# Kernel tuning notes

Measured on AMD Instinct MI355X. Metric: run time of the kernel, lower is better.

## Reference

```python
import jax, jax.numpy as jnp
import numpy as np
import math

B, T, C, H = 4, 2048, 512, 8
HD = C // H


def make_alibias(block_size, ms):
    # ALiBi-style per-head bias: -m_h * |i - j|, shape [1, H, S, S]
    idx = jnp.arange(block_size)
    dist = jnp.abs(idx[:, None] - idx[None, :]).astype(jnp.float32)  # [S,S]
    return -ms[None, :, None, None] * dist[None, None, :, :]


def setup_inputs() -> dict:
    key = jax.random.key(0)
    k1, k2, k3, k4, k5 = jax.random.split(key, 5)
    x = jax.random.normal(k1, (B, T, C), dtype=jnp.float32)
    Wqkv = jax.random.normal(k2, (C, 3 * C), dtype=jnp.float32) * (1.0 / math.sqrt(C))
    bqkv = jax.random.normal(k3, (3 * C,), dtype=jnp.float32) * 0.02
    Wproj = jax.random.normal(k4, (C, C), dtype=jnp.float32) * (1.0 / math.sqrt(C))
    bproj = jax.random.normal(k5, (C,), dtype=jnp.float32) * 0.02
    ms = jnp.arange(1, H + 1, dtype=jnp.float32) * 0.05
    alibias = make_alibias(T, ms)  # [1,H,T,T]
    return {"x": x, "Wqkv": Wqkv, "bqkv": bqkv, "Wproj": Wproj, "bproj": bproj, "alibias": alibias}


def reference(x, Wqkv, bqkv, Wproj, bproj, alibias):
    Bv, Tv, Cv = x.shape
    qkv = x @ Wqkv + bqkv                      # [B,T,3C]
    q, k, v = jnp.split(qkv, 3, axis=-1)
    # [B,T,C] -> [B,H,T,hd]
    def heads(t):
        return t.reshape(Bv, Tv, H, HD).transpose(0, 2, 1, 3)
    q, k, v = heads(q), heads(k), heads(v)
    att = jnp.einsum('bhqd,bhkd->bhqk', q, k) * (1.0 / math.sqrt(HD))
    att = att + alibias[:, :, :Tv, :Tv]
    att = jax.nn.softmax(att, axis=-1)
    y = jnp.einsum('bhqk,bhkd->bhqd', att, v)  # [B,H,T,hd]
    y = y.transpose(0, 2, 1, 3).reshape(Bv, Tv, Cv)
    return y @ Wproj + bproj
```

## Files before the change

kernel.cpp:

```cpp
#include <hip/hip_runtime.h>
#include <hip/hip_bf16.h>

#define LOG2E 1.4426950408889634f

typedef __attribute__((ext_vector_type(8))) short short8;
typedef __attribute__((ext_vector_type(8))) __bf16 bf16x8;
typedef __attribute__((ext_vector_type(4))) float f32x4;

__device__ __forceinline__ unsigned short f2b(float f){
  unsigned int u = __builtin_bit_cast(unsigned int, f);
  u += 0x7fffu + ((u >> 16) & 1u);
  return (unsigned short)(u >> 16);
}

__device__ __forceinline__ unsigned int cvtpk(float lo, float hi){
  unsigned int r;
  asm("v_cvt_pk_bf16_f32 %0, %1, %2" : "=v"(r) : "v"(lo), "v"(hi));
  return r;
}

__device__ __forceinline__ void gload16(const void* g, void* l){
  __builtin_amdgcn_global_load_lds(
      (const __attribute__((address_space(1))) unsigned int*)g,
      (__attribute__((address_space(3))) unsigned int*)l, 16, 0, 0);
}

__global__ __launch_bounds__(256) void prep_kernel(
    const float* __restrict__ x, const float* __restrict__ Wqkv, const float* __restrict__ Wproj,
    unsigned short* __restrict__ xb, unsigned short* __restrict__ wqkvT, unsigned short* __restrict__ wprojT){
  __shared__ unsigned short T[64][72];
  const int bid = blockIdx.x, tid = threadIdx.x;
  if (bid < 2048){
    size_t i = ((size_t)bid * 256 + tid) * 8;
    float4 a = *(const float4*)(x + i);
    float4 b = *(const float4*)(x + i + 4);
    short8 s;
    s[0]=(short)f2b(a.x); s[1]=(short)f2b(a.y); s[2]=(short)f2b(a.z); s[3]=(short)f2b(a.w);
    s[4]=(short)f2b(b.x); s[5]=(short)f2b(b.y); s[6]=(short)f2b(b.z); s[7]=(short)f2b(b.w);
    *(short8*)(xb + i) = s;
    return;
  }
  const float* in; unsigned short* out; int R, C, bx, by;
  if (bid < 2240){ int t = bid - 2048; bx = t % 24; by = t / 24; in = Wqkv; out = wqkvT; R = 512; C = 1536; }
  else           { int t = bid - 2240; bx = t % 8;  by = t / 8;  in = Wproj; out = wprojT; R = 512; C = 512; }
  const int r0 = by * 64, c0 = bx * 64;
  {
    const int i = tid >> 2, jg = (tid & 3) * 16;
    const float* src = in + (size_t)(r0 + i) * C + c0 + jg;
    #pragma unroll
    for (int e = 0; e < 16; e += 4){
      float4 v = *(const float4*)(src + e);
      T[i][jg + e + 0] = f2b(v.x);
      T[i][jg + e + 1] = f2b(v.y);
      T[i][jg + e + 2] = f2b(v.z);
      T[i][jg + e + 3] = f2b(v.w);
    }
  }
  __syncthreads();
  {
    const int j = tid >> 2, ig = (tid & 3) * 16;
    short8 w0, w1;
    #pragma unroll
    for (int e = 0; e < 8; e++) w0[e] = (short)T[ig + e][j];
    #pragma unroll
    for (int e = 0; e < 8; e++) w1[e] = (short)T[ig + 8 + e][j];
    unsigned short* dst = out + (size_t)(c0 + j) * R + r0 + ig;
    *(short8*)dst = w0;
    *(short8*)(dst + 8) = w1;
  }
}

__global__ __launch_bounds__(256,2) void gemm_qkv_kernel(
    const unsigned short* __restrict__ A,
    const unsigned short* __restrict__ Bt,
    const float* __restrict__ bias,
    unsigned short* __restrict__ Qb,
    unsigned short* __restrict__ Kb,
    unsigned short* __restrict__ VTb,
    float* __restrict__ Mq, float* __restrict__ Mk){
  __shared__ unsigned short As[128*64];
  __shared__ unsigned short Bs[128*64];
  const int tid = threadIdx.x, wid = tid >> 6, lane = tid & 63;
  const int wr = wid >> 1, wc = wid & 1;
  const int fr = lane & 15, fq = lane >> 4;
  const int fr7 = fr & 7;
  const int bm = blockIdx.x * 128, bn = blockIdx.y * 128;
  f32x4 acc[4][4];
  #pragma unroll
  for (int m=0;m<4;m++)
    #pragma unroll
    for (int n=0;n<4;n++) acc[m][n] = (f32x4){0.f,0.f,0.f,0.f};

  for (int k0 = 0; k0 < 512; k0 += 64){
    __syncthreads();
    #pragma unroll
    for (int it=0; it<4; it++){
      const int s = it*256 + tid;
      const int row = s >> 3, c = s & 7;
      const int sc = c ^ (row & 7);
      void* al = (void*)(As + (it*256 + wid*64)*8);
      void* bl = (void*)(Bs + (it*256 + wid*64)*8);
      gload16(A  + (size_t)(bm + row)*512 + k0 + sc*8, al);
      gload16(Bt + (size_t)(bn + row)*512 + k0 + sc*8, bl);
    }
    __syncthreads();
    bf16x8 af[4][2], bfv[4][2];
    #pragma unroll
    for (int m=0;m<4;m++)
      #pragma unroll
      for (int kk=0;kk<2;kk++)
        af[m][kk]  = *(const bf16x8*)&As[(wr*64 + m*16 + fr)*64 + (((kk*4+fq)^fr7)*8)];
    #pragma unroll
    for (int n=0;n<4;n++)
      #pragma unroll
      for (int kk=0;kk<2;kk++)
        bfv[n][kk] = *(const bf16x8*)&Bs[(wc*64 + n*16 + fr)*64 + (((kk*4+fq)^fr7)*8)];
    #pragma unroll
    for (int kk=0;kk<2;kk++)
      #pragma unroll
      for (int m=0;m<4;m++)
        #pragma unroll
        for (int n=0;n<4;n++)
          acc[m][n] = __builtin_amdgcn_mfma_f32_16x16x32_bf16(af[m][kk], bfv[n][kk], acc[m][n], 0,0,0);
  }

  const float SCQ = 0.125f * LOG2E;
  const int colbase = bn + wc*64;
  const int which = colbase >> 9;
  float ss[4][4];
  #pragma unroll
  for (int m=0;m<4;m++)
    #pragma unroll
    for (int g=0;g<4;g++) ss[m][g] = 0.f;

  #pragma unroll
  for (int m=0;m<4;m++){
    const int row0 = bm + wr*64 + m*16 + fq*4;
    const int b_ = row0 >> 11, t_ = row0 & 2047;
    #pragma unroll
    for (int n=0;n<4;n++){
      const int col = colbase + n*16 + fr;
      const int c = col & 511, hh = c >> 6, dd = c & 63;
      const float bv = bias[col];
      if (which == 0){
        #pragma unroll
        for (int g=0; g<4; g++){
          const float v = (acc[m][n][g] + bv) * SCQ;
          ss[m][g] = fmaf(v, v, ss[m][g]);
          Qb[((size_t)(b_*8 + hh)*2048 + t_ + g)*64 + dd] = f2b(v);
        }
      } else if (which == 1){
        #pragma unroll
        for (int g=0; g<4; g++){
          const float v = acc[m][n][g] + bv;
          ss[m][g] = fmaf(v, v, ss[m][g]);
          Kb[((size_t)(b_*8 + hh)*2048 + t_ + g)*64 + dd] = f2b(v);
        }
      } else {
        uint2 pk;
        pk.x = cvtpk(acc[m][n][0] + bv, acc[m][n][1] + bv);
        pk.y = cvtpk(acc[m][n][2] + bv, acc[m][n][3] + bv);
        *(uint2*)&VTb[((size_t)(b_*8 + hh)*64 + dd)*2048 + t_] = pk;
      }
    }
  }

  if (which <= 1){
    #pragma unroll
    for (int m=0;m<4;m++)
      #pragma unroll
      for (int g=0;g<4;g++){
        float s = ss[m][g];
        s += __shfl_xor(s, 1); s += __shfl_xor(s, 2);
        s += __shfl_xor(s, 4); s += __shfl_xor(s, 8);
        ss[m][g] = s;
      }
    float mx = 0.f;
    #pragma unroll
    for (int m=0;m<4;m++)
      #pragma unroll
      for (int g=0;g<4;g++) mx = fmaxf(mx, ss[m][g]);
    mx = fmaxf(mx, __shfl_xor(mx, 16));
    mx = fmaxf(mx, __shfl_xor(mx, 32));
    if (lane == 0){
      const int rowbase = bm + wr*64;
      const int b_ = rowbase >> 11, qc_ = (rowbase >> 6) & 31;
      const int h_ = (colbase >> 6) & 7;
      float* M = which ? Mk : Mq;
      M[(b_*8 + h_)*32 + qc_] = sqrtf(mx) * 1.01f;
    }
  }
}

__global__ __launch_bounds__(256,2) void attn_kernel(
    const unsigned short* __restrict__ Q,
    const unsigned short* __restrict__ K,
    const unsigned short* __restrict__ VT,
    const float* __restrict__ alib,
    const float* __restrict__ Mqa,
    const float* __restrict__ Mka,
    unsigned short* __restrict__ Y){
  __shared__ unsigned short Ks[2][64*64];
  __shared__ unsigned short Vs[2][64*64];
  __shared__ unsigned short Ps[4][16][72];
  __shared__ float MkS[32];
  __shared__ float wred[4];
  __shared__ int lst[32];
  __shared__ int nsh;
  const int tid = threadIdx.x, wid = tid >> 6, lane = tid & 63;
  const int fr = lane & 15, fq = lane >> 4;
  const int fr7 = fr & 7;
  const int id = blockIdx.x;
  const int h = id >> 7, r_ = id & 127, b = r_ >> 5, qc = r_ & 31;
  const int bh = b*8 + h;
  const int q0 = qc*64 + wid*16;
  const unsigned short* Qp = Q  + (size_t)bh * 131072;
  const unsigned short* Kp = K  + (size_t)bh * 131072;
  const unsigned short* Vp = VT + (size_t)bh * 131072;
  const float nmh2 = alib[(size_t)h * 4194304 + 1] * LOG2E;
  const float MqMk0 = Mqa[bh*32 + qc];
  if (tid < 32) MkS[tid] = Mka[bh*32 + tid];

  bf16x8 qf[2];
  #pragma unroll
  for (int kk=0;kk<2;kk++)
    qf[kk] = *(const bf16x8*)(Qp + (size_t)(q0 + fr)*64 + kk*32 + fq*8);

  f32x4 o[4];
  #pragma unroll
  for (int ni=0;ni<4;ni++) o[ni] = (f32x4){0.f,0.f,0.f,0.f};
  float mr = -1e30f, lr = 0.f;
  const float qi = (float)(q0 + fr);
  const float qb = nmh2 * qi;
  f32x4 ka[4];
  #pragma unroll
  for (int ni=0;ni<4;ni++)
    #pragma unroll
    for (int g=0;g<4;g++) ka[ni][g] = nmh2 * (float)(ni*16 + fq*4 + g);

  auto stage = [&](int kt, int buf){
    const int kb = kt * 64;
    #pragma unroll
    for (int it=0; it<2; it++){
      const int s = it*256 + tid;
      const int row = s >> 3, c = s & 7;
      const int sc = c ^ (row & 7);
      gload16(Kp + (size_t)(kb + row)*64 + sc*8, (void*)(Ks[buf] + (it*256 + wid*64)*8));
      gload16(Vp + (size_t)row*2048 + kb + sc*8, (void*)(Vs[buf] + (it*256 + wid*64)*8));
    }
  };

  auto compute = [&](int kt, int buf, bool diag){
    const int kb = kt * 64;
    const unsigned short* KsB = Ks[buf];
    const unsigned short* VsB = Vs[buf];
    bf16x8 kf[4][2], vf[4][2];
    #pragma unroll
    for (int ni=0;ni<4;ni++)
      #pragma unroll
      for (int kk=0;kk<2;kk++){
        const int r = ni*16 + fr;
        const int sw = ((kk*4 + fq) ^ fr7) * 8;
        kf[ni][kk] = *(const bf16x8*)&KsB[r*64 + sw];
        vf[ni][kk] = *(const bf16x8*)&VsB[r*64 + sw];
      }

    f32x4 st[4];
    const f32x4 fz = {0.f,0.f,0.f,0.f};
    #pragma unroll
    for (int ni=0;ni<4;ni++){
      f32x4 t0 = __builtin_amdgcn_mfma_f32_16x16x32_bf16(kf[ni][0], qf[0], fz, 0,0,0);
      st[ni] = __builtin_amdgcn_mfma_f32_16x16x32_bf16(kf[ni][1], qf[1], t0, 0,0,0);
    }

    float cadd;
    if (diag){
      const float base = qi - (float)(kb + fq*4);
      #pragma unroll
      for (int ni=0;ni<4;ni++)
        #pragma unroll
        for (int g=0;g<4;g++){
          const float d = fabsf(base - (float)(ni*16 + g));
          st[ni][g] = fmaf(nmh2, d, st[ni][g]);
        }
      cadd = 0.f;
    } else {
      const float s1 = (kt > qc) ? 1.f : -1.f;
      #pragma unroll
      for (int ni=0;ni<4;ni++)
        #pragma unroll
        for (int g=0;g<4;g++)
          st[ni][g] = fmaf(s1, ka[ni][g], st[ni][g]);
      cadd = s1 * (nmh2 * (float)kb - qb);
    }

    float m0 = fmaxf(fmaxf(st[0][0], st[0][1]), fmaxf(st[0][2], st[0][3]));
    float m1 = fmaxf(fmaxf(st[1][0], st[1][1]), fmaxf(st[1][2], st[1][3]));
    float m2 = fmaxf(fmaxf(st[2][0], st[2][1]), fmaxf(st[2][2], st[2][3]));
    float m3 = fmaxf(fmaxf(st[3][0], st[3][1]), fmaxf(st[3][2], st[3][3]));
    float tm = fmaxf(fmaxf(m0, m1), fmaxf(m2, m3));
    tm = fmaxf(tm, __shfl_xor(tm, 16));
    tm = fmaxf(tm, __shfl_xor(tm, 32));
    const float tmt = tm + cadd;

    const bool nog = __all(tmt <= mr);
    float mn, sc;
    if (nog){
      mn = mr;
    } else {
      mn = fmaxf(mr, tmt);
      sc = exp2f(mr - mn);
      mr = mn;
    }
    const float mexp = mn - cadd;
    float rs = 0.f;
    #pragma unroll
    for (int ni=0;ni<4;ni++){
      #pragma unroll
      for (int g=0;g<4;g++){
        const float p = exp2f(st[ni][g] - mexp);
        st[ni][g] = p;
        rs += p;
      }
    }
    rs += __shfl_xor(rs, 16);
    rs += __shfl_xor(rs, 32);
    if (nog){
      lr += rs;
    } else {
      lr = lr*sc + rs;
      #pragma unroll
      for (int g=0;g<4;g++){
        const float sv = __shfl(sc, fq*4 + g);
        #pragma unroll
        for (int ni=0;ni<4;ni++) o[ni][g] *= sv;
      }
    }
    #pragma unroll
    for (int ni=0;ni<4;ni++){
      uint2 pk;
      pk.x = cvtpk(st[ni][0], st[ni][1]);
      pk.y = cvtpk(st[ni][2], st[ni][3]);
      *(uint2*)&Ps[wid][fr][ni*16 + fq*4] = pk;
    }

    bf16x8 pf[2];
    #pragma unroll
    for (int kk=0;kk<2;kk++)
      pf[kk] = *(const bf16x8*)&Ps[wid][fr][kk*32 + fq*8];
    #pragma unroll
    for (int ni=0;ni<4;ni++){
      o[ni] = __builtin_amdgcn_mfma_f32_16x16x32_bf16(pf[0], vf[ni][0], o[ni], 0,0,0);
      o[ni] = __builtin_amdgcn_mfma_f32_16x16x32_bf16(pf[1], vf[ni][1], o[ni], 0,0,0);
    }
  };

  stage(qc, 0);
  asm volatile("s_waitcnt vmcnt(0)" ::: "memory");
  __builtin_amdgcn_sched_barrier(0);
  __builtin_amdgcn_s_barrier();
  compute(qc, 0, true);

  {
    float m = mr;
    #pragma unroll
    for (int d=1; d<16; d<<=1) m = fminf(m, __shfl_xor(m, d));
    if (lane == 0) wred[wid] = m;
  }
  __syncthreads();
  const float thresh = fminf(fminf(wred[0], wred[1]), fminf(wred[2], wred[3])) - 16.0f;

  if (tid == 0){
    float maxMk = 0.f;
    #pragma unroll
    for (int t=0; t<32; t++) maxMk = fmaxf(maxMk, MkS[t]);
    int n = 0;
    for (int dt = 1; dt < 32; dt++){
      const float biasmax = nmh2 * (float)((dt - 1)*64 + 1);
      if (MqMk0 * maxMk + biasmax < thresh) break;
      int kt = qc + dt;
      if (kt < 32 && MqMk0 * MkS[kt] + biasmax >= thresh) lst[n++] = kt;
      kt = qc - dt;
      if (kt >= 0 && MqMk0 * MkS[kt] + biasmax >= thresh) lst[n++] = kt;
    }
    nsh = n;
  }
  __syncthreads();
  const int n = nsh;

  if (n > 0){
    stage(lst[0], 1);
    for (int j = 0; j < n; j++){
      asm volatile("s_waitcnt lgkmcnt(0)" ::: "memory");
      __builtin_amdgcn_sched_barrier(0);
      __builtin_amdgcn_s_barrier();
      if (j + 1 < n){
        stage(lst[j+1], j & 1);
        asm volatile("s_waitcnt vmcnt(4)" ::: "memory");
      } else {
        asm volatile("s_waitcnt vmcnt(0)" ::: "memory");
      }
      __builtin_amdgcn_sched_barrier(0);
      __builtin_amdgcn_s_barrier();
      compute(lst[j], (j+1)&1, false);
    }
  }

  {
    const float inv = 1.0f / lr;
    #pragma unroll
    for (int g=0;g<4;g++){
      const float iv = __shfl(inv, fq*4 + g);
      const int t = q0 + fq*4 + g;
      #pragma unroll
      for (int ni=0;ni<4;ni++)
        Y[(size_t)(b*2048 + t)*512 + h*64 + ni*16 + fr] = f2b(o[ni][g] * iv);
    }
  }
}

__global__ __launch_bounds__(256,2) void gemm_proj_kernel(
    const unsigned short* __restrict__ A,
    const unsigned short* __restrict__ Bt,
    const float* __restrict__ bias,
    float* __restrict__ out){
  __shared__ unsigned short As[128*64];
  __shared__ unsigned short Bs[128*64];
  const int tid = threadIdx.x, wid = tid >> 6, lane = tid & 63;
  const int wr = wid >> 1, wc = wid & 1;
  const int fr = lane & 15, fq = lane >> 4;
  const int fr7 = fr & 7;
  const int bm = blockIdx.x * 128, bn = blockIdx.y * 128;
  f32x4 acc[4][4];
  #pragma unroll
  for (int m=0;m<4;m++)
    #pragma unroll
    for (int n=0;n<4;n++) acc[m][n] = (f32x4){0.f,0.f,0.f,0.f};

  for (int k0 = 0; k0 < 512; k0 += 64){
    __syncthreads();
    #pragma unroll
    for (int it=0; it<4; it++){
      const int s = it*256 + tid;
      const int row = s >> 3, c = s & 7;
      const int sc = c ^ (row & 7);
      void* al = (void*)(As + (it*256 + wid*64)*8);
      void* bl = (void*)(Bs + (it*256 + wid*64)*8);
      gload16(A  + (size_t)(bm + row)*512 + k0 + sc*8, al);
      gload16(Bt + (size_t)(bn + row)*512 + k0 + sc*8, bl);
    }
    __syncthreads();
    bf16x8 af[4][2], bfv[4][2];
    #pragma unroll
    for (int m=0;m<4;m++)
      #pragma unroll
      for (int kk=0;kk<2;kk++)
        af[m][kk]  = *(const bf16x8*)&As[(wr*64 + m*16 + fr)*64 + (((kk*4+fq)^fr7)*8)];
    #pragma unroll
    for (int n=0;n<4;n++)
      #pragma unroll
      for (int kk=0;kk<2;kk++)
        bfv[n][kk] = *(const bf16x8*)&Bs[(wc*64 + n*16 + fr)*64 + (((kk*4+fq)^fr7)*8)];
    #pragma unroll
    for (int kk=0;kk<2;kk++)
      #pragma unroll
      for (int m=0;m<4;m++)
        #pragma unroll
        for (int n=0;n<4;n++)
          acc[m][n] = __builtin_amdgcn_mfma_f32_16x16x32_bf16(af[m][kk], bfv[n][kk], acc[m][n], 0,0,0);
  }

  #pragma unroll
  for (int m=0;m<4;m++){
    const int row0 = bm + wr*64 + m*16 + fq*4;
    #pragma unroll
    for (int n=0;n<4;n++){
      const int col = bn + wc*64 + n*16 + fr;
      const float bv = bias[col];
      #pragma unroll
      for (int g=0; g<4; g++)
        out[(size_t)(row0 + g)*512 + col] = acc[m][n][g] + bv;
    }
  }
}

extern "C" void kernel_launch(void* const* d_in, const int* in_sizes, int n_in,
                              void* d_out, int out_size, void* d_ws, size_t ws_size,
                              hipStream_t stream){
  const float* x     = (const float*)d_in[0];
  const float* Wqkv  = (const float*)d_in[1];
  const float* bqkv  = (const float*)d_in[2];
  const float* Wproj = (const float*)d_in[3];
  const float* bproj = (const float*)d_in[4];
  const float* alib  = (const float*)d_in[5];
  char* ws = (char*)d_ws;
  unsigned short* xb     = (unsigned short*)(ws);
  unsigned short* wqkvT  = (unsigned short*)(ws + 8388608);
  unsigned short* wprojT = (unsigned short*)(ws + 9961472);
  unsigned short* Qb     = (unsigned short*)(ws + 10485760);
  unsigned short* Kb     = (unsigned short*)(ws + 18874368);
  unsigned short* VTb    = (unsigned short*)(ws + 27262976);
  unsigned short* Yb     = (unsigned short*)(ws + 35651584);
  float* out = (float*)d_out;
  float* Mq = out + 4194304 - 2048;
  float* Mk = Mq + 1024;

  prep_kernel<<<2304, 256, 0, stream>>>(x, Wqkv, Wproj, xb, wqkvT, wprojT);
  gemm_qkv_kernel<<<dim3(64, 12), 256, 0, stream>>>(xb, wqkvT, bqkv, Qb, Kb, VTb, Mq, Mk);
  attn_kernel<<<1024, 256, 0, stream>>>(Qb, Kb, VTb, alib, Mq, Mk, Yb);
  gemm_proj_kernel<<<dim3(64, 4), 256, 0, stream>>>(Yb, wprojT, bproj, out);
}
```

Measured before the change: 70.90 us.

## Compute softmax row sums via MFMA with ones and add per-wave tile skipping

```diff
diff --git a/kernel.cpp b/kernel.cpp
--- a/kernel.cpp
+++ b/kernel.cpp
@@ -192,7 +192,7 @@
   }
 }
 
-__global__ __launch_bounds__(256,2) void attn_kernel(
+__global__ __launch_bounds__(256,3) void attn_kernel(
     const unsigned short* __restrict__ Q,
     const unsigned short* __restrict__ K,
     const unsigned short* __restrict__ VT,
@@ -226,10 +226,15 @@
   for (int kk=0;kk<2;kk++)
     qf[kk] = *(const bf16x8*)(Qp + (size_t)(q0 + fr)*64 + kk*32 + fq*8);
 
-  f32x4 o[4];
+  bf16x8 ones;
+  #pragma unroll
+  for (int e=0;e<8;e++) ones[e] = __builtin_bit_cast(__bf16, (unsigned short)0x3F80);
+
+  f32x4 o[4], osum;
   #pragma unroll
   for (int ni=0;ni<4;ni++) o[ni] = (f32x4){0.f,0.f,0.f,0.f};
-  float mr = -1e30f, lr = 0.f;
+  osum = (f32x4){0.f,0.f,0.f,0.f};
+  float mr = -1e30f;
   const float qi = (float)(q0 + fr);
   const float qb = nmh2 * qi;
   f32x4 ka[4];
@@ -304,36 +309,26 @@
     const float tmt = tm + cadd;
 
     const bool nog = __all(tmt <= mr);
-    float mn, sc;
-    if (nog){
-      mn = mr;
-    } else {
+    float mn = mr, sc;
+    if (!nog){
       mn = fmaxf(mr, tmt);
       sc = exp2f(mr - mn);
       mr = mn;
     }
     const float mexp = mn - cadd;
-    float rs = 0.f;
-    #pragma unroll
-    for (int ni=0;ni<4;ni++){
-      #pragma unroll
-      for (int g=0;g<4;g++){
-        const float p = exp2f(st[ni][g] - mexp);
-        st[ni][g] = p;
-        rs += p;
-      }
-    }
-    rs += __shfl_xor(rs, 16);
-    rs += __shfl_xor(rs, 32);
-    if (nog){
-      lr += rs;
-    } else {
-      lr = lr*sc + rs;
+    #pragma unroll
+    for (int ni=0;ni<4;ni++)
+      #pragma unroll
+      for (int g=0;g<4;g++)
+        st[ni][g] = exp2f(st[ni][g] - mexp);
+
+    if (!nog){
       #pragma unroll
       for (int g=0;g<4;g++){
         const float sv = __shfl(sc, fq*4 + g);
         #pragma unroll
         for (int ni=0;ni<4;ni++) o[ni][g] *= sv;
+        osum[g] *= sv;
       }
     }
     #pragma unroll
@@ -353,6 +348,8 @@
       o[ni] = __builtin_amdgcn_mfma_f32_16x16x32_bf16(pf[0], vf[ni][0], o[ni], 0,0,0);
       o[ni] = __builtin_amdgcn_mfma_f32_16x16x32_bf16(pf[1], vf[ni][1], o[ni], 0,0,0);
     }
+    osum = __builtin_amdgcn_mfma_f32_16x16x32_bf16(pf[0], ones, osum, 0,0,0);
+    osum = __builtin_amdgcn_mfma_f32_16x16x32_bf16(pf[1], ones, osum, 0,0,0);
   };
 
   stage(qc, 0);
@@ -361,14 +358,13 @@
   __builtin_amdgcn_s_barrier();
   compute(qc, 0, true);
 
-  {
-    float m = mr;
-    #pragma unroll
-    for (int d=1; d<16; d<<=1) m = fminf(m, __shfl_xor(m, d));
-    if (lane == 0) wred[wid] = m;
-  }
+  float wm = mr;
+  #pragma unroll
+  for (int d=1; d<16; d<<=1) wm = fminf(wm, __shfl_xor(wm, d));
+  if (lane == 0) wred[wid] = wm;
   __syncthreads();
-  const float thresh = fminf(fminf(wred[0], wred[1]), fminf(wred[2], wred[3])) - 16.0f;
+  const float thresh  = fminf(fminf(wred[0], wred[1]), fminf(wred[2], wred[3])) - 14.0f;
+  const float threshW = wm - 14.0f;
 
   if (tid == 0){
     float maxMk = 0.f;
@@ -402,20 +398,20 @@
       }
       __builtin_amdgcn_sched_barrier(0);
       __builtin_amdgcn_s_barrier();
-      compute(lst[j], (j+1)&1, false);
-    }
-  }
-
-  {
-    const float inv = 1.0f / lr;
-    #pragma unroll
-    for (int g=0;g<4;g++){
-      const float iv = __shfl(inv, fq*4 + g);
-      const int t = q0 + fq*4 + g;
-      #pragma unroll
-      for (int ni=0;ni<4;ni++)
-        Y[(size_t)(b*2048 + t)*512 + h*64 + ni*16 + fr] = f2b(o[ni][g] * iv);
-    }
+      const int kt = lst[j];
+      const int dminW = (kt > qc) ? (kt*64 - (q0 + 15)) : (q0 - (kt*64 + 63));
+      if (MqMk0 * MkS[kt] + nmh2 * (float)dminW >= threshW)
+        compute(kt, (j+1)&1, false);
+    }
+  }
+
+  #pragma unroll
+  for (int g=0;g<4;g++){
+    const float iv = 1.0f / osum[g];
+    const int t = q0 + fq*4 + g;
+    #pragma unroll
+    for (int ni=0;ni<4;ni++)
+      Y[(size_t)(b*2048 + t)*512 + h*64 + ni*16 + fr] = f2b(o[ni][g] * iv);
   }
 }
 
```

Result: faster. 68.98 us (-2.7%).
